# Kernel optimization log

Measured on AMD Instinct MI355X. Metric: run time of the kernel, lower is better.

The kernel has to match this reference:

```python
import jax, jax.numpy as jnp
import numpy as np

H = 128        # hidden_dim
R = 50         # num_rbf
L = 4          # num_layers
CUTOFF = 5.0
N = 10000      # atoms
M = 64         # molecules
BOX = 54.7     # box side -> ~32 neighbors within cutoff
EPS = 1e-5     # LayerNorm eps (torch default)


def setup_inputs() -> dict:
    rng = np.random.default_rng(0)
    positions = rng.uniform(0.0, BOX, size=(N, 3)).astype(np.float32)
    # static radius graph (the torch module filters a dense NxN pair list by cutoff;
    # we do that once here so runtime shapes are fixed / jit-friendly)
    sq = (positions ** 2).sum(-1)
    d2 = sq[:, None] + sq[None, :] - 2.0 * positions @ positions.T
    mask = (d2 < CUTOFF * CUTOFF) & ~np.eye(N, dtype=bool)
    row, col = np.nonzero(mask)
    edge_index = jnp.asarray(np.stack([row, col]).astype(np.int32))  # [2, E]

    key = jax.random.key(0)
    ks = jax.random.split(key, 6)
    s = 0.05
    return dict(
        atomic_numbers=jax.random.randint(ks[0], (N,), 0, 100),
        positions=jnp.asarray(positions),
        batch=jnp.asarray((np.arange(N) * M // N).astype(np.int32)),  # sorted, all M present
        edge_index=edge_index,
        embedding=jax.random.normal(ks[1], (100, H), jnp.float32) * s,
        W1=jax.random.normal(ks[2], (L, H + R, H), jnp.float32) * s,
        b1=jnp.zeros((L, H), jnp.float32),
        W2=jax.random.normal(ks[3], (L, H, H), jnp.float32) * s,
        b2=jnp.zeros((L, H), jnp.float32),
        W_ih=jax.random.normal(ks[4], (L, H, 3 * H), jnp.float32) * s,
        b_ih=jax.random.normal(ks[5], (L, 3 * H), jnp.float32) * s,
        b_hh=jnp.zeros((L, 3 * H), jnp.float32),
        ln_g=jnp.ones((H,), jnp.float32),
        ln_b=jnp.zeros((H,), jnp.float32),
    )


def reference(atomic_numbers, positions, batch, edge_index, embedding,
              W1, b1, W2, b2, W_ih, b_ih, b_hh, ln_g, ln_b):
    x = embedding[jnp.clip(atomic_numbers, 0, 99)]                  # [N, H]
    row, col = edge_index[0], edge_index[1]
    d = jnp.linalg.norm(positions[row] - positions[col], axis=-1)   # [E]
    centers = jnp.linspace(0.0, CUTOFF, R)
    width = CUTOFF / R
    rbf = jnp.exp(-((d[:, None] - centers) ** 2) / (2.0 * width * width))  # [E, R]
    n_atoms = x.shape[0]
    for l in range(L):
        x_j = x[row]                                                # gather [E, H]
        inp = jnp.concatenate([x_j, rbf], axis=-1)                  # [E, H+R]
        msg = jax.nn.silu(inp @ W1[l] + b1[l]) @ W2[l] + b2[l]      # [E, H]
        aggr = jax.ops.segment_sum(msg, col, num_segments=n_atoms)  # [N, H]
        # GRU step with h0 = 0: W_hh @ h vanishes, only b_hh survives
        gi = aggr @ W_ih[l] + b_ih[l]                               # [N, 3H]
        gi_r, gi_z, gi_n = jnp.split(gi, 3, axis=-1)
        bh_r, bh_z, bh_n = jnp.split(b_hh[l], 3)
        r = jax.nn.sigmoid(gi_r + bh_r)
        z = jax.nn.sigmoid(gi_z + bh_z)
        n = jnp.tanh(gi_n + r * bh_n)
        x = x + (1.0 - z) * n                                       # h' = (1-z)*n + z*0
    mu = x.mean(-1, keepdims=True)
    var = ((x - mu) ** 2).mean(-1, keepdims=True)
    x = (x - mu) / jnp.sqrt(var + EPS) * ln_g + ln_b
    sums = jax.ops.segment_sum(x, batch, num_segments=M)            # [M, H]
    counts = jax.ops.segment_sum(jnp.ones((x.shape[0],), jnp.float32), batch, num_segments=M)
    graph_rep = sums / jnp.clip(counts, 1.0)[:, None]
    return x, graph_rep
```

## Files before the change

kernel.cpp:

```cpp
#include <hip/hip_runtime.h>
#include <hip/hip_bf16.h>
#include <math.h>


#define HH 128
#define RR 50
#define LL 4
#define L2E 1.4426950408889634f

typedef __attribute__((ext_vector_type(8))) short short8;
typedef __attribute__((ext_vector_type(4))) float floatx4;

__device__ __forceinline__ unsigned short f2bf(float f) {
    unsigned u = __float_as_uint(f);
    unsigned r = (u + 0x7fffu + ((u >> 16) & 1u)) >> 16;
    return (unsigned short)r;
}
__device__ __forceinline__ unsigned pack_bf2(float lo, float hi) {
    unsigned u0 = __float_as_uint(lo) + 0x8000u;
    unsigned u1 = __float_as_uint(hi) + 0x8000u;
    return __builtin_amdgcn_perm(u1, u0, 0x07060302);
}
__device__ __forceinline__ float fast_sigmoid(float x) {
    return __builtin_amdgcn_rcpf(1.f + __builtin_amdgcn_exp2f(x * (-L2E)));
}
__device__ __forceinline__ float fast_tanh(float x) {
    x = fminf(fmaxf(x, -15.f), 15.f);
    float t = __builtin_amdgcn_exp2f(x * (2.f * L2E));
    return (t - 1.f) * __builtin_amdgcn_rcpf(t + 1.f);
}
__device__ __forceinline__ int imin(int a, int b) { return a < b ? a : b; }

__global__ __launch_bounds__(256) void prep_kernel(
    const int* __restrict__ an, const float* __restrict__ emb,
    float* __restrict__ X,
    const float* __restrict__ pos, const int* __restrict__ erow,
    const int* __restrict__ ecol, float* __restrict__ dist,
    int* __restrict__ rowptr, int* __restrict__ bptr,
    const int* __restrict__ batch,
    const float* __restrict__ W1, unsigned short* __restrict__ W1rT,
    unsigned short* __restrict__ W1xT,
    const float* __restrict__ W2, const float* __restrict__ Wih,
    unsigned short* __restrict__ WcT,
    const float* __restrict__ b2, float* __restrict__ P,
    const float* __restrict__ b1, unsigned short* __restrict__ embWbf,
    int* __restrict__ zc, float* __restrict__ outg,
    int N, int E, int M)
{
    int gidx = blockIdx.x * 256 + threadIdx.x;
    int c0 = N * HH;
    if (gidx < c0) {
        int i = gidx >> 7, n = gidx & 127;
        int z = an[i];
        z = z < 0 ? 0 : (z > 99 ? 99 : z);
        X[gidx] = emb[z * HH + n];
        return;
    }
    gidx -= c0;
    int PT = E > N ? E : N;
    if (gidx < PT) {
        int i = gidx;
        if (i < E) {
            int rc = erow[i];
            int rp = (i > 0) ? erow[i - 1] : -1;
            for (int r = rp + 1; r <= rc; ++r) rowptr[r] = i;
            if (i == E - 1)
                for (int r = rc + 1; r <= N; ++r) rowptr[r] = E;
        }
        if (i < N) {
            int bc = batch[i];
            int bp = (i > 0) ? batch[i - 1] : -1;
            for (int m = bp + 1; m <= bc; ++m) bptr[m] = i;
            if (i == N - 1)
                for (int m = bc + 1; m <= M; ++m) bptr[m] = N;
        }
        return;
    }
    gidx -= PT;
    if (gidx < E) {
        int e = gidx;
        int r = erow[e], c = ecol[e];
        float dx = pos[r * 3 + 0] - pos[c * 3 + 0];
        float dy = pos[r * 3 + 1] - pos[c * 3 + 1];
        float dz = pos[r * 3 + 2] - pos[c * 3 + 2];
        dist[e] = sqrtf(dx * dx + dy * dy + dz * dz);
        return;
    }
    gidx -= E;
    if (gidx < LL * HH * 64) {
        int l = gidx >> 13, rem = gidx & 8191;
        int f = rem >> 9, lane2 = (rem >> 3) & 63, j = rem & 7;
        int nt = f >> 1, h = f & 1;
        int n = nt * 16 + (lane2 & 15);
        int k = h * 32 + (lane2 >> 4) * 8 + j;
        float v = (k < RR) ? W1[((size_t)l * 178 + 128 + k) * HH + n] : 0.f;
        W1rT[gidx] = f2bf(v);
        return;
    }
    gidx -= LL * HH * 64;
    if (gidx < LL * HH * HH) {
        int l = gidx >> 14, rem = gidx & 16383, n = rem >> 7, k = rem & 127;
        W1xT[gidx] = f2bf(W1[((size_t)l * 178 + k) * HH + n]);
        return;
    }
    gidx -= LL * HH * HH;
    if (gidx < LL * HH * 384) {
        int l = gidx / (HH * 384), rem = gidx % (HH * 384);
        int i = rem / 384, j = rem % 384;
        const float* w2row = W2 + ((size_t)l * HH + i) * HH;
        const float* wih = Wih + (size_t)l * HH * 384;
        float acc = 0.f;
#pragma unroll 4
        for (int k = 0; k < HH; ++k)
            acc = fmaf(w2row[k], wih[(size_t)k * 384 + j], acc);
        WcT[((size_t)l * 384 + j) * HH + i] = f2bf(acc);
        return;
    }
    gidx -= LL * HH * 384;
    if (gidx < LL * 384) {
        int l = gidx / 384, j = gidx % 384;
        const float* b2l = b2 + (size_t)l * HH;
        const float* wih = Wih + (size_t)l * HH * 384;
        float acc = 0.f;
#pragma unroll 4
        for (int k = 0; k < HH; ++k)
            acc = fmaf(b2l[k], wih[(size_t)k * 384 + j], acc);
        P[gidx] = acc;
        return;
    }
    gidx -= LL * 384;
    if (gidx < N) {
        int z = an[gidx];
        zc[gidx] = z < 0 ? 0 : (z > 99 ? 99 : z);
        return;
    }
    gidx -= N;
    if (gidx < 100 * HH) {
        int z = gidx >> 7, n = gidx & 127;
        const float* er = emb + (size_t)z * HH;
        float acc = b1[n];
#pragma unroll 4
        for (int k = 0; k < HH; ++k)
            acc = fmaf(er[k], W1[(size_t)k * HH + n], acc);
        embWbf[gidx] = f2bf(acc);
        return;
    }
    gidx -= 100 * HH;
    if (gidx < M * HH) {
        outg[gidx] = 0.f;
    }
}

__global__ __launch_bounds__(256) void edge_mfma_kernel(
    const unsigned short* __restrict__ Xsrc, const unsigned short* __restrict__ W1rTf,
    const float* __restrict__ dist, const int* __restrict__ rowptr,
    const int* __restrict__ ecol, const int* __restrict__ zc, int use_z,
    unsigned short* __restrict__ Sbf, int N, int nwaves)
{
    __shared__ __align__(16) unsigned short W1s[8192];
    int tid = threadIdx.x;
    {
        const uint4* src = (const uint4*)W1rTf;
        uint4* dst = (uint4*)W1s;
#pragma unroll
        for (int i = 0; i < 4; ++i) dst[tid + i * 256] = src[tid + i * 256];
    }
    __syncthreads();

    int wid = (blockIdx.x << 2) + (tid >> 6);
    int lane = tid & 63;
    int c = lane & 15, q = lane >> 4;

    const float stepc = 5.0f / 49.0f;
    const float negc = -50.f * L2E;
    float kqs = (float)(q << 3) * stepc;

    int NW = 2 * N;
    for (int w = wid; w < NW; w += nwaves) {
        int a = w >> 1, h = w & 1;
        int es = rowptr[a], ee = rowptr[a + 1];
        float acc[4][4];
#pragma unroll
        for (int t = 0; t < 4; ++t)
#pragma unroll
            for (int r = 0; r < 4; ++r) acc[t][r] = 0.f;

        if (es < ee) {
            int last = ee - 1;
            int ce0 = imin(es + c, last);
            float dcur = dist[ce0];
            int c0raw = ecol[ce0];
            int rowcur = use_z ? zc[c0raw] : c0raw;
            int ce1 = imin(es + 16 + c, last);
            float dnxt = dist[ce1];
            int colnxt = ecol[ce1];

            for (int eb = es; eb < ee; eb += 16) {
                const unsigned short* xwrow = Xsrc + (size_t)rowcur * HH + h * 64;
                uint2 gx[4];
#pragma unroll
                for (int t = 0; t < 4; ++t)
                    gx[t] = *(const uint2*)&xwrow[t * 16 + (q << 2)];

                float d_t = dcur;
                dcur = dnxt;
                int rownxt = use_z ? zc[colnxt] : colnxt;
                int ce2 = imin(eb + 32 + c, last);
                dnxt = dist[ce2];
                colnxt = ecol[ce2];
                rowcur = rownxt;

                float dq0 = d_t - kqs;
                float dq1 = dq0 - 32.f * stepc;
                union { unsigned u[4]; short8 s; } ub0, ub1;
#pragma unroll
                for (int p = 0; p < 4; ++p) {
                    float t0 = dq0 - (float)(2 * p) * stepc;
                    float t1 = dq0 - (float)(2 * p + 1) * stepc;
                    float e0f = __builtin_amdgcn_exp2f(negc * t0 * t0);
                    float e1f = __builtin_amdgcn_exp2f(negc * t1 * t1);
                    ub0.u[p] = pack_bf2(e0f, e1f);
                    float t2 = dq1 - (float)(2 * p) * stepc;
                    float t3 = dq1 - (float)(2 * p + 1) * stepc;
                    float e2f = __builtin_amdgcn_exp2f(negc * t2 * t2);
                    float e3f = __builtin_amdgcn_exp2f(negc * t3 * t3);
                    ub1.u[p] = pack_bf2(e2f, e3f);
                }
                short8 B0 = ub0.s, B1 = ub1.s;
                float msk = ((eb + c) < ee) ? 1.f : 0.f;

                unsigned wbyte = (unsigned)(lane * 16);
                asm volatile("" : "+v"(wbyte));
                const char* Wlp = (const char*)W1s + wbyte;

#pragma unroll
                for (int t = 0; t < 4; ++t) {
                    int f0 = (h * 4 + t) * 2;
                    short8 A0 = *(const short8*)(Wlp + f0 * 1024);
                    short8 A1 = *(const short8*)(Wlp + (f0 + 1) * 1024);
                    floatx4 C;
                    C[0] = __uint_as_float(gx[t].x << 16);
                    C[1] = __uint_as_float(gx[t].x & 0xffff0000u);
                    C[2] = __uint_as_float(gx[t].y << 16);
                    C[3] = __uint_as_float(gx[t].y & 0xffff0000u);
                    C = __builtin_amdgcn_mfma_f32_16x16x32_bf16(A0, B0, C, 0, 0, 0);
                    C = __builtin_amdgcn_mfma_f32_16x16x32_bf16(A1, B1, C, 0, 0, 0);
#pragma unroll
                    for (int r = 0; r < 4; ++r) {
                        float hh = C[r];
                        float v = hh * fast_sigmoid(hh);
                        acc[t][r] = fmaf(v, msk, acc[t][r]);
                    }
                }
            }
        }

        int b0 = c & 1, b1 = (c >> 1) & 1, b2 = (c >> 2) & 1, b3 = (c >> 3) & 1;
        float s1[4][2];
#pragma unroll
        for (int t = 0; t < 4; ++t)
#pragma unroll
            for (int p = 0; p < 2; ++p) {
                float keep = b0 ? acc[t][2 * p + 1] : acc[t][2 * p];
                float send = b0 ? acc[t][2 * p] : acc[t][2 * p + 1];
                s1[t][p] = keep + __shfl_xor(send, 1, 64);
            }
        float s2[4];
#pragma unroll
        for (int t = 0; t < 4; ++t) {
            float keep = b1 ? s1[t][1] : s1[t][0];
            float send = b1 ? s1[t][0] : s1[t][1];
            s2[t] = keep + __shfl_xor(send, 2, 64);
        }
        float s3[2];
#pragma unroll
        for (int u = 0; u < 2; ++u) {
            float keep = b2 ? s2[2 * u + 1] : s2[2 * u];
            float send = b2 ? s2[2 * u] : s2[2 * u + 1];
            s3[u] = keep + __shfl_xor(send, 4, 64);
        }
        float keep = b3 ? s3[1] : s3[0];
        float send = b3 ? s3[0] : s3[1];
        float fin = keep + __shfl_xor(send, 8, 64);

        int t_fin = 2 * b3 + b2;
        int r_fin = 2 * b1 + b0;
        int n = t_fin * 16 + (q << 2) + r_fin;
        Sbf[(size_t)a * HH + h * 64 + n] = f2bf(fin);
    }
}

#define GA 32
__global__ __launch_bounds__(256) void grux_mfma_kernel(
    const unsigned short* __restrict__ Sbf, const unsigned short* __restrict__ WcT,
    const float* __restrict__ P, const float* __restrict__ bih,
    const float* __restrict__ bhh, const int* __restrict__ rowptr,
    float* __restrict__ X, int N,
    const unsigned short* __restrict__ W1xT, const float* __restrict__ b1next,
    unsigned short* __restrict__ XWb, int do_xw,
    int do_ln, const float* __restrict__ lng, const float* __restrict__ lnb,
    const int* __restrict__ batch, const int* __restrict__ bptr,
    float* __restrict__ outx, float* __restrict__ outg)
{
    __shared__ __align__(16) union ShMem {
        struct { unsigned short Sb[GA][136]; unsigned short Xb[GA][136]; } s;
        struct { float Xf[GA][132]; float pool[2][HH]; } f;
    } u;
    unsigned short (&Sb)[GA][136] = u.s.Sb;
    unsigned short (&Xb)[GA][136] = u.s.Xb;
    float (&Xf)[GA][132] = u.f.Xf;
    float (&pool)[2][HH] = u.f.pool;

    int tid = threadIdx.x;
    int abase = blockIdx.x * GA;
    int w = tid >> 6, lane = tid & 63, c = lane & 15, q = lane >> 4;

    float pn[2][3], bi[2][3], bh[2][3], deg[2][4];
#pragma unroll
    for (int t = 0; t < 2; ++t) {
        int n = w * 32 + t * 16 + c;
#pragma unroll
        for (int g = 0; g < 3; ++g) {
            pn[t][g] = P[g * 128 + n];
            bi[t][g] = bih[g * 128 + n];
            bh[t][g] = bhh[g * 128 + n];
        }
    }
#pragma unroll
    for (int sub = 0; sub < 2; ++sub)
#pragma unroll
        for (int r = 0; r < 4; ++r) {
            int a = abase + sub * 16 + q * 4 + r;
            deg[sub][r] = (a < N) ? (float)(rowptr[a + 1] - rowptr[a]) : 0.f;
        }

    {
        int a = tid >> 3, ch = tid & 7;
        int aa = abase + a; if (aa >= N) aa = N - 1;
        const uint4* src = (const uint4*)(Sbf + (size_t)aa * HH + ch * 16);
        uint4 v0 = src[0];
        uint4 v1 = src[1];
        uint4* dst = (uint4*)&Sb[a][ch * 16];
        dst[0] = v0;
        dst[1] = v1;
    }
    __syncthreads();

    floatx4 Cg[3][2][2];
#pragma unroll
    for (int g = 0; g < 3; ++g)
#pragma unroll
        for (int t = 0; t < 2; ++t)
#pragma unroll
            for (int sub = 0; sub < 2; ++sub)
                Cg[g][t][sub] = floatx4{0.f, 0.f, 0.f, 0.f};

#pragma unroll
    for (int kt = 0; kt < 4; ++kt) {
        short8 A0 = *(const short8*)&Sb[c][kt * 32 + q * 8];
        short8 A1 = *(const short8*)&Sb[16 + c][kt * 32 + q * 8];
#pragma unroll
        for (int g = 0; g < 3; ++g)
#pragma unroll
            for (int t = 0; t < 2; ++t) {
                int nrow = g * 128 + w * 32 + t * 16 + c;
                short8 B = *(const short8*)&WcT[(size_t)nrow * HH + kt * 32 + q * 8];
                Cg[g][t][0] = __builtin_amdgcn_mfma_f32_16x16x32_bf16(A0, B, Cg[g][t][0], 0, 0, 0);
                Cg[g][t][1] = __builtin_amdgcn_mfma_f32_16x16x32_bf16(A1, B, Cg[g][t][1], 0, 0, 0);
            }
    }

    if (do_ln) __syncthreads();

#pragma unroll
    for (int sub = 0; sub < 2; ++sub)
#pragma unroll
        for (int r = 0; r < 4; ++r) {
            int am = sub * 16 + q * 4 + r;
            int a = abase + am;
            bool ok = a < N;
#pragma unroll
            for (int t = 0; t < 2; ++t) {
                int n = w * 32 + t * 16 + c;
                float g0 = Cg[0][t][sub][r] + deg[sub][r] * pn[t][0] + bi[t][0];
                float g1 = Cg[1][t][sub][r] + deg[sub][r] * pn[t][1] + bi[t][1];
                float g2 = Cg[2][t][sub][r] + deg[sub][r] * pn[t][2] + bi[t][2];
                float rr = fast_sigmoid(g0 + bh[t][0]);
                float zz = fast_sigmoid(g1 + bh[t][1]);
                float nn = fast_tanh(g2 + rr * bh[t][2]);
                float xv = 0.f;
                if (ok) {
                    xv = X[(size_t)a * HH + n] + (1.f - zz) * nn;
                    if (!do_ln) X[(size_t)a * HH + n] = xv;
                }
                if (do_ln) Xf[am][n] = xv;
                else       Xb[am][n] = f2bf(xv);
            }
        }

    if (do_ln) {
        (&pool[0][0])[tid] = 0.f;
        __syncthreads();

        int row = tid >> 3, j = tid & 7;
        int a2 = abase + row;
        float4 x0 = *(const float4*)&Xf[row][j * 16];
        float4 x1 = *(const float4*)&Xf[row][j * 16 + 4];
        float4 x2 = *(const float4*)&Xf[row][j * 16 + 8];
        float4 x3 = *(const float4*)&Xf[row][j * 16 + 12];
        float s = x0.x + x0.y + x0.z + x0.w + x1.x + x1.y + x1.z + x1.w
                + x2.x + x2.y + x2.z + x2.w + x3.x + x3.y + x3.z + x3.w;
        s += __shfl_xor(s, 1, 64);
        s += __shfl_xor(s, 2, 64);
        s += __shfl_xor(s, 4, 64);
        float mu = s * (1.f / 128.f);
        float qv = 0.f;
#define QACC(v) { float dx=(v).x-mu, dy=(v).y-mu, dz=(v).z-mu, dw=(v).w-mu; \
                  qv += dx*dx + dy*dy + dz*dz + dw*dw; }
        QACC(x0) QACC(x1) QACC(x2) QACC(x3)
#undef QACC
        qv += __shfl_xor(qv, 1, 64);
        qv += __shfl_xor(qv, 2, 64);
        qv += __shfl_xor(qv, 4, 64);
        float inv = rsqrtf(qv * (1.f / 128.f) + 1e-5f);

        int m0 = batch[abase];
        if (a2 < N) {
            int midx = batch[a2] - m0;
            const float4* gg = (const float4*)&lng[j * 16];
            const float4* bb = (const float4*)&lnb[j * 16];
            float* outrow = outx + (size_t)a2 * HH + j * 16;
            float* pl = &pool[midx][j * 16];
            float4 xs[4] = {x0, x1, x2, x3};
#pragma unroll
            for (int i = 0; i < 4; ++i) {
                float4 gv = gg[i], bv = bb[i], xv4 = xs[i];
                float4 y;
                y.x = (xv4.x - mu) * inv * gv.x + bv.x;
                y.y = (xv4.y - mu) * inv * gv.y + bv.y;
                y.z = (xv4.z - mu) * inv * gv.z + bv.z;
                y.w = (xv4.w - mu) * inv * gv.w + bv.w;
                *(float4*)(outrow + i * 4) = y;
                atomicAdd(pl + i * 4 + 0, y.x);
                atomicAdd(pl + i * 4 + 1, y.y);
                atomicAdd(pl + i * 4 + 2, y.z);
                atomicAdd(pl + i * 4 + 3, y.w);
            }
        }
        __syncthreads();

        int a_last = abase + GA - 1; if (a_last >= N) a_last = N - 1;
        int mlast = batch[a_last];
        int mi = tid >> 7, col = tid & 127;
        int m = m0 + mi;
        if (m <= mlast) {
            float cnt = (float)(bptr[m + 1] - bptr[m]);
            float invc = 1.f / fmaxf(cnt, 1.f);
            atomicAdd(&outg[(size_t)m * HH + col], pool[mi][col] * invc);
        }
        return;
    }

    if (!do_xw) return;
    __syncthreads();

    floatx4 Cx[2][2];
#pragma unroll
    for (int t = 0; t < 2; ++t)
#pragma unroll
        for (int sub = 0; sub < 2; ++sub)
            Cx[t][sub] = floatx4{0.f, 0.f, 0.f, 0.f};
#pragma unroll
    for (int kt = 0; kt < 4; ++kt) {
        short8 A0 = *(const short8*)&Xb[c][kt * 32 + q * 8];
        short8 A1 = *(const short8*)&Xb[16 + c][kt * 32 + q * 8];
#pragma unroll
        for (int t = 0; t < 2; ++t) {
            int nrow = w * 32 + t * 16 + c;
            short8 B = *(const short8*)&W1xT[(size_t)nrow * HH + kt * 32 + q * 8];
            Cx[t][0] = __builtin_amdgcn_mfma_f32_16x16x32_bf16(A0, B, Cx[t][0], 0, 0, 0);
            Cx[t][1] = __builtin_amdgcn_mfma_f32_16x16x32_bf16(A1, B, Cx[t][1], 0, 0, 0);
        }
    }
#pragma unroll
    for (int sub = 0; sub < 2; ++sub)
#pragma unroll
        for (int r = 0; r < 4; ++r) {
            int a = abase + sub * 16 + q * 4 + r;
            if (a >= N) continue;
#pragma unroll
            for (int t = 0; t < 2; ++t) {
                int n = w * 32 + t * 16 + c;
                XWb[(size_t)a * HH + n] = f2bf(Cx[t][sub][r] + b1next[n]);
            }
        }
}

extern "C" void kernel_launch(void* const* d_in, const int* in_sizes, int n_in,
                              void* d_out, int out_size, void* d_ws, size_t ws_size,
                              hipStream_t stream)
{
    const int*   an   = (const int*)d_in[0];
    const float* pos  = (const float*)d_in[1];
    const int*   bat  = (const int*)d_in[2];
    const int*   eidx = (const int*)d_in[3];
    const float* emb  = (const float*)d_in[4];
    const float* W1   = (const float*)d_in[5];
    const float* b1   = (const float*)d_in[6];
    const float* W2   = (const float*)d_in[7];
    const float* b2   = (const float*)d_in[8];
    const float* Wih  = (const float*)d_in[9];
    const float* bih  = (const float*)d_in[10];
    const float* bhh  = (const float*)d_in[11];
    const float* lng  = (const float*)d_in[12];
    const float* lnb  = (const float*)d_in[13];

    int N = in_sizes[0];
    int E = in_sizes[3] / 2;
    int M = out_size / HH - N;
    const int* erow = eidx;
    const int* ecol = eidx + E;

    float* ws   = (float*)d_ws;
    size_t off = 0;
    float* X    = ws + off; off += (size_t)N * HH;
    unsigned short* Sbf = (unsigned short*)(ws + off); off += (size_t)N * HH / 2;
    unsigned short* XWb = (unsigned short*)(ws + off); off += (size_t)N * HH / 2;
    float* P    = ws + off; off += LL * 384;
    float* dist = ws + off; off += E;
    int* rowptr = (int*)(ws + off); off += N + 1;
    int* bptr   = (int*)(ws + off); off += M + 1;
    off = (off + 3) & ~(size_t)3;
    unsigned short* W1rT = (unsigned short*)(ws + off); off += (size_t)LL * HH * 32;
    unsigned short* W1xT = (unsigned short*)(ws + off); off += (size_t)LL * HH * 64;
    unsigned short* WcT  = (unsigned short*)(ws + off); off += (size_t)LL * 384 * 64;
    unsigned short* embWbf = (unsigned short*)(ws + off); off += (size_t)100 * HH / 2;
    int* zc     = (int*)(ws + off); off += N;

    float* outx = (float*)d_out;
    float* outg = outx + (size_t)N * HH;

    int PT = (E > N ? E : N);
    long total = (long)N * HH + PT + E + LL * HH * 64 + LL * HH * HH
               + LL * HH * 384 + LL * 384 + N + 100 * HH + (long)M * HH;
    int prep_blocks = (int)((total + 255) / 256);

    prep_kernel<<<prep_blocks, 256, 0, stream>>>(
        an, emb, X, pos, erow, ecol, dist, rowptr, bptr, bat,
        W1, W1rT, W1xT, W2, Wih, WcT, b2, P,
        b1, embWbf, zc, outg, N, E, M);

    int eblocks = (2 * N + 3) / 4;
    int nwaves = eblocks * 4;
    int grux_blocks = (N + GA - 1) / GA;
    for (int l = 0; l < LL; ++l) {
        edge_mfma_kernel<<<eblocks, 256, 0, stream>>>(
            (l == 0) ? embWbf : XWb, W1rT + (size_t)l * HH * 64,
            dist, rowptr, ecol, zc, (l == 0) ? 1 : 0, Sbf, N, nwaves);
        int do_xw = (l < LL - 1) ? 1 : 0;
        int do_ln = (l == LL - 1) ? 1 : 0;
        int ln = (l + 1 < LL) ? l + 1 : l;
        grux_mfma_kernel<<<grux_blocks, 256, 0, stream>>>(
            Sbf, WcT + (size_t)l * 384 * HH, P + l * 384,
            bih + l * 384, bhh + l * 384, rowptr, X, N,
            W1xT + (size_t)ln * HH * HH, b1 + (size_t)ln * HH, XWb, do_xw,
            do_ln, lng, lnb, bat, bptr, outx, outg);
    }
}
```

Measured before the change: 305.5 us.

## Fuse edge message kernel and GRU update into one per-layer kernel

Merges the per-atom edge aggregation kernel and the GRU/next-layer projection kernel into a single layer kernel that processes 16 atoms per block. Aggregated messages now stay in shared memory instead of round-tripping through a global bf16 buffer. XW output is double-buffered across layers so a layer can read the previous projection while writing the next. The cost is smaller GRU MFMA tiles (16 atoms instead of 32), which halves reuse of the WcT/W1xT loads from global memory. Every block also reloads the W1 slice into shared memory, and there are 8 wave-tasks per block over 4 waves, which can cause load imbalance.

```diff
diff --git a/kernel.cpp b/kernel.cpp
--- a/kernel.cpp
+++ b/kernel.cpp
@@ -6,6 +6,7 @@
 #define HH 128
 #define RR 50
 #define LL 4
+#define GA 16
 #define L2E 1.4426950408889634f
 
 typedef __attribute__((ext_vector_type(8))) short short8;
@@ -151,13 +152,29 @@
     }
 }
 
-__global__ __launch_bounds__(256) void edge_mfma_kernel(
+__global__ __launch_bounds__(256) void layer_kernel(
     const unsigned short* __restrict__ Xsrc, const unsigned short* __restrict__ W1rTf,
     const float* __restrict__ dist, const int* __restrict__ rowptr,
     const int* __restrict__ ecol, const int* __restrict__ zc, int use_z,
-    unsigned short* __restrict__ Sbf, int N, int nwaves)
+    const unsigned short* __restrict__ WcT, const float* __restrict__ P,
+    const float* __restrict__ bih, const float* __restrict__ bhh,
+    float* __restrict__ X, int N,
+    const unsigned short* __restrict__ W1xT, const float* __restrict__ b1next,
+    unsigned short* __restrict__ XWout, int do_xw,
+    int do_ln, const float* __restrict__ lng, const float* __restrict__ lnb,
+    const int* __restrict__ batch, const int* __restrict__ bptr,
+    float* __restrict__ outx, float* __restrict__ outg)
 {
     __shared__ __align__(16) unsigned short W1s[8192];
+    __shared__ __align__(16) union ShMem {
+        struct { unsigned short Sb[GA][136]; unsigned short Xb[GA][136]; } s;
+        struct { float Xf[GA][132]; float pool[2][HH]; } f;
+    } sh;
+    unsigned short (&Sb)[GA][136] = sh.s.Sb;
+    unsigned short (&Xb)[GA][136] = sh.s.Xb;
+    float (&Xf)[GA][132] = sh.f.Xf;
+    float (&pool)[2][HH] = sh.f.pool;
+
     int tid = threadIdx.x;
     {
         const uint4* src = (const uint4*)W1rTf;
@@ -167,18 +184,20 @@
     }
     __syncthreads();
 
-    int wid = (blockIdx.x << 2) + (tid >> 6);
-    int lane = tid & 63;
+    int abase = blockIdx.x * GA;
+    int wavei = tid >> 6, lane = tid & 63;
     int c = lane & 15, q = lane >> 4;
 
     const float stepc = 5.0f / 49.0f;
     const float negc = -50.f * L2E;
     float kqs = (float)(q << 3) * stepc;
 
-    int NW = 2 * N;
-    for (int w = wid; w < NW; w += nwaves) {
-        int a = w >> 1, h = w & 1;
-        int es = rowptr[a], ee = rowptr[a + 1];
+#pragma unroll 1
+    for (int uu = wavei; uu < 2 * GA; uu += 4) {
+        int a_loc = uu >> 1, h = uu & 1;
+        int a = abase + a_loc;
+        int es = 0, ee = 0;
+        if (a < N) { es = rowptr[a]; ee = rowptr[a + 1]; }
         float acc[4][4];
 #pragma unroll
         for (int t = 0; t < 4; ++t)
@@ -247,8 +266,8 @@
                     C = __builtin_amdgcn_mfma_f32_16x16x32_bf16(A1, B1, C, 0, 0, 0);
 #pragma unroll
                     for (int r = 0; r < 4; ++r) {
-                        float hh = C[r];
-                        float v = hh * fast_sigmoid(hh);
+                        float hh2 = C[r];
+                        float v = hh2 * fast_sigmoid(hh2);
                         acc[t][r] = fmaf(v, msk, acc[t][r]);
                     }
                 }
@@ -274,10 +293,10 @@
         }
         float s3[2];
 #pragma unroll
-        for (int u = 0; u < 2; ++u) {
-            float keep = b2 ? s2[2 * u + 1] : s2[2 * u];
-            float send = b2 ? s2[2 * u] : s2[2 * u + 1];
-            s3[u] = keep + __shfl_xor(send, 4, 64);
+        for (int u2 = 0; u2 < 2; ++u2) {
+            float keep = b2 ? s2[2 * u2 + 1] : s2[2 * u2];
+            float send = b2 ? s2[2 * u2] : s2[2 * u2 + 1];
+            s3[u2] = keep + __shfl_xor(send, 4, 64);
         }
         float keep = b3 ? s3[1] : s3[0];
         float send = b3 ? s3[0] : s3[1];
@@ -286,39 +305,15 @@
         int t_fin = 2 * b3 + b2;
         int r_fin = 2 * b1 + b0;
         int n = t_fin * 16 + (q << 2) + r_fin;
-        Sbf[(size_t)a * HH + h * 64 + n] = f2bf(fin);
-    }
-}
-
-#define GA 32
-__global__ __launch_bounds__(256) void grux_mfma_kernel(
-    const unsigned short* __restrict__ Sbf, const unsigned short* __restrict__ WcT,
-    const float* __restrict__ P, const float* __restrict__ bih,
-    const float* __restrict__ bhh, const int* __restrict__ rowptr,
-    float* __restrict__ X, int N,
-    const unsigned short* __restrict__ W1xT, const float* __restrict__ b1next,
-    unsigned short* __restrict__ XWb, int do_xw,
-    int do_ln, const float* __restrict__ lng, const float* __restrict__ lnb,
-    const int* __restrict__ batch, const int* __restrict__ bptr,
-    float* __restrict__ outx, float* __restrict__ outg)
-{
-    __shared__ __align__(16) union ShMem {
-        struct { unsigned short Sb[GA][136]; unsigned short Xb[GA][136]; } s;
-        struct { float Xf[GA][132]; float pool[2][HH]; } f;
-    } u;
-    unsigned short (&Sb)[GA][136] = u.s.Sb;
-    unsigned short (&Xb)[GA][136] = u.s.Xb;
-    float (&Xf)[GA][132] = u.f.Xf;
-    float (&pool)[2][HH] = u.f.pool;
-
-    int tid = threadIdx.x;
-    int abase = blockIdx.x * GA;
-    int w = tid >> 6, lane = tid & 63, c = lane & 15, q = lane >> 4;
-
-    float pn[2][3], bi[2][3], bh[2][3], deg[2][4];
+        Sb[a_loc][h * 64 + n] = f2bf(fin);
+    }
+    __syncthreads();
+
+    int wq = wavei;
+    float pn[2][3], bi[2][3], bh[2][3], deg[4];
 #pragma unroll
     for (int t = 0; t < 2; ++t) {
-        int n = w * 32 + t * 16 + c;
+        int n = wq * 32 + t * 16 + c;
 #pragma unroll
         for (int g = 0; g < 3; ++g) {
             pn[t][g] = P[g * 128 + n];
@@ -327,113 +322,92 @@
         }
     }
 #pragma unroll
-    for (int sub = 0; sub < 2; ++sub)
-#pragma unroll
-        for (int r = 0; r < 4; ++r) {
-            int a = abase + sub * 16 + q * 4 + r;
-            deg[sub][r] = (a < N) ? (float)(rowptr[a + 1] - rowptr[a]) : 0.f;
-        }
-
-    {
-        int a = tid >> 3, ch = tid & 7;
-        int aa = abase + a; if (aa >= N) aa = N - 1;
-        const uint4* src = (const uint4*)(Sbf + (size_t)aa * HH + ch * 16);
-        uint4 v0 = src[0];
-        uint4 v1 = src[1];
-        uint4* dst = (uint4*)&Sb[a][ch * 16];
-        dst[0] = v0;
-        dst[1] = v1;
-    }
-    __syncthreads();
-
-    floatx4 Cg[3][2][2];
+    for (int r = 0; r < 4; ++r) {
+        int a = abase + q * 4 + r;
+        deg[r] = (a < N) ? (float)(rowptr[a + 1] - rowptr[a]) : 0.f;
+    }
+
+    floatx4 Cg[3][2];
 #pragma unroll
     for (int g = 0; g < 3; ++g)
 #pragma unroll
         for (int t = 0; t < 2; ++t)
-#pragma unroll
-            for (int sub = 0; sub < 2; ++sub)
-                Cg[g][t][sub] = floatx4{0.f, 0.f, 0.f, 0.f};
+            Cg[g][t] = floatx4{0.f, 0.f, 0.f, 0.f};
 
 #pragma unroll
     for (int kt = 0; kt < 4; ++kt) {
         short8 A0 = *(const short8*)&Sb[c][kt * 32 + q * 8];
-        short8 A1 = *(const short8*)&Sb[16 + c][kt * 32 + q * 8];
 #pragma unroll
         for (int g = 0; g < 3; ++g)
 #pragma unroll
             for (int t = 0; t < 2; ++t) {
-                int nrow = g * 128 + w * 32 + t * 16 + c;
+                int nrow = g * 128 + wq * 32 + t * 16 + c;
                 short8 B = *(const short8*)&WcT[(size_t)nrow * HH + kt * 32 + q * 8];
-                Cg[g][t][0] = __builtin_amdgcn_mfma_f32_16x16x32_bf16(A0, B, Cg[g][t][0], 0, 0, 0);
-                Cg[g][t][1] = __builtin_amdgcn_mfma_f32_16x16x32_bf16(A1, B, Cg[g][t][1], 0, 0, 0);
+                Cg[g][t] = __builtin_amdgcn_mfma_f32_16x16x32_bf16(A0, B, Cg[g][t], 0, 0, 0);
             }
     }
 
     if (do_ln) __syncthreads();
 
 #pragma unroll
-    for (int sub = 0; sub < 2; ++sub)
-#pragma unroll
-        for (int r = 0; r < 4; ++r) {
-            int am = sub * 16 + q * 4 + r;
-            int a = abase + am;
-            bool ok = a < N;
-#pragma unroll
-            for (int t = 0; t < 2; ++t) {
-                int n = w * 32 + t * 16 + c;
-                float g0 = Cg[0][t][sub][r] + deg[sub][r] * pn[t][0] + bi[t][0];
-                float g1 = Cg[1][t][sub][r] + deg[sub][r] * pn[t][1] + bi[t][1];
-                float g2 = Cg[2][t][sub][r] + deg[sub][r] * pn[t][2] + bi[t][2];
-                float rr = fast_sigmoid(g0 + bh[t][0]);
-                float zz = fast_sigmoid(g1 + bh[t][1]);
-                float nn = fast_tanh(g2 + rr * bh[t][2]);
-                float xv = 0.f;
-                if (ok) {
-                    xv = X[(size_t)a * HH + n] + (1.f - zz) * nn;
-                    if (!do_ln) X[(size_t)a * HH + n] = xv;
-                }
-                if (do_ln) Xf[am][n] = xv;
-                else       Xb[am][n] = f2bf(xv);
+    for (int r = 0; r < 4; ++r) {
+        int am = q * 4 + r;
+        int a = abase + am;
+        bool ok = a < N;
+#pragma unroll
+        for (int t = 0; t < 2; ++t) {
+            int n = wq * 32 + t * 16 + c;
+            float g0 = Cg[0][t][r] + deg[r] * pn[t][0] + bi[t][0];
+            float g1 = Cg[1][t][r] + deg[r] * pn[t][1] + bi[t][1];
+            float g2 = Cg[2][t][r] + deg[r] * pn[t][2] + bi[t][2];
+            float rr = fast_sigmoid(g0 + bh[t][0]);
+            float zz = fast_sigmoid(g1 + bh[t][1]);
+            float nn = fast_tanh(g2 + rr * bh[t][2]);
+            float xv = 0.f;
+            if (ok) {
+                xv = X[(size_t)a * HH + n] + (1.f - zz) * nn;
+                if (!do_ln) X[(size_t)a * HH + n] = xv;
             }
-        }
+            if (do_ln) Xf[am][n] = xv;
+            else       Xb[am][n] = f2bf(xv);
+        }
+    }
 
     if (do_ln) {
         (&pool[0][0])[tid] = 0.f;
         __syncthreads();
 
-        int row = tid >> 3, j = tid & 7;
+        int row = tid >> 4, j = tid & 15;
         int a2 = abase + row;
-        float4 x0 = *(const float4*)&Xf[row][j * 16];
-        float4 x1 = *(const float4*)&Xf[row][j * 16 + 4];
-        float4 x2 = *(const float4*)&Xf[row][j * 16 + 8];
-        float4 x3 = *(const float4*)&Xf[row][j * 16 + 12];
-        float s = x0.x + x0.y + x0.z + x0.w + x1.x + x1.y + x1.z + x1.w
-                + x2.x + x2.y + x2.z + x2.w + x3.x + x3.y + x3.z + x3.w;
+        float4 x0 = *(const float4*)&Xf[row][j * 8];
+        float4 x1 = *(const float4*)&Xf[row][j * 8 + 4];
+        float s = x0.x + x0.y + x0.z + x0.w + x1.x + x1.y + x1.z + x1.w;
         s += __shfl_xor(s, 1, 64);
         s += __shfl_xor(s, 2, 64);
         s += __shfl_xor(s, 4, 64);
+        s += __shfl_xor(s, 8, 64);
         float mu = s * (1.f / 128.f);
         float qv = 0.f;
 #define QACC(v) { float dx=(v).x-mu, dy=(v).y-mu, dz=(v).z-mu, dw=(v).w-mu; \
                   qv += dx*dx + dy*dy + dz*dz + dw*dw; }
-        QACC(x0) QACC(x1) QACC(x2) QACC(x3)
+        QACC(x0) QACC(x1)
 #undef QACC
         qv += __shfl_xor(qv, 1, 64);
         qv += __shfl_xor(qv, 2, 64);
         qv += __shfl_xor(qv, 4, 64);
+        qv += __shfl_xor(qv, 8, 64);
         float inv = rsqrtf(qv * (1.f / 128.f) + 1e-5f);
 
         int m0 = batch[abase];
         if (a2 < N) {
             int midx = batch[a2] - m0;
-            const float4* gg = (const float4*)&lng[j * 16];
-            const float4* bb = (const float4*)&lnb[j * 16];
-            float* outrow = outx + (size_t)a2 * HH + j * 16;
-            float* pl = &pool[midx][j * 16];
-            float4 xs[4] = {x0, x1, x2, x3};
-#pragma unroll
-            for (int i = 0; i < 4; ++i) {
+            const float4* gg = (const float4*)&lng[j * 8];
+            const float4* bb = (const float4*)&lnb[j * 8];
+            float* outrow = outx + (size_t)a2 * HH + j * 8;
+            float* pl = &pool[midx][j * 8];
+            float4 xs[2] = {x0, x1};
+#pragma unroll
+            for (int i = 0; i < 2; ++i) {
                 float4 gv = gg[i], bv = bb[i], xv4 = xs[i];
                 float4 y;
                 y.x = (xv4.x - mu) * inv * gv.x + bv.x;
@@ -464,36 +438,30 @@
     if (!do_xw) return;
     __syncthreads();
 
-    floatx4 Cx[2][2];
+    floatx4 Cx[2];
 #pragma unroll
     for (int t = 0; t < 2; ++t)
-#pragma unroll
-        for (int sub = 0; sub < 2; ++sub)
-            Cx[t][sub] = floatx4{0.f, 0.f, 0.f, 0.f};
+        Cx[t] = floatx4{0.f, 0.f, 0.f, 0.f};
 #pragma unroll
     for (int kt = 0; kt < 4; ++kt) {
         short8 A0 = *(const short8*)&Xb[c][kt * 32 + q * 8];
-        short8 A1 = *(const short8*)&Xb[16 + c][kt * 32 + q * 8];
 #pragma unroll
         for (int t = 0; t < 2; ++t) {
-            int nrow = w * 32 + t * 16 + c;
+            int nrow = wq * 32 + t * 16 + c;
             short8 B = *(const short8*)&W1xT[(size_t)nrow * HH + kt * 32 + q * 8];
-            Cx[t][0] = __builtin_amdgcn_mfma_f32_16x16x32_bf16(A0, B, Cx[t][0], 0, 0, 0);
-            Cx[t][1] = __builtin_amdgcn_mfma_f32_16x16x32_bf16(A1, B, Cx[t][1], 0, 0, 0);
-        }
-    }
-#pragma unroll
-    for (int sub = 0; sub < 2; ++sub)
-#pragma unroll
-        for (int r = 0; r < 4; ++r) {
-            int a = abase + sub * 16 + q * 4 + r;
-            if (a >= N) continue;
-#pragma unroll
-            for (int t = 0; t < 2; ++t) {
-                int n = w * 32 + t * 16 + c;
-                XWb[(size_t)a * HH + n] = f2bf(Cx[t][sub][r] + b1next[n]);
-            }
-        }
+            Cx[t] = __builtin_amdgcn_mfma_f32_16x16x32_bf16(A0, B, Cx[t], 0, 0, 0);
+        }
+    }
+#pragma unroll
+    for (int r = 0; r < 4; ++r) {
+        int a = abase + q * 4 + r;
+        if (a >= N) continue;
+#pragma unroll
+        for (int t = 0; t < 2; ++t) {
+            int n = wq * 32 + t * 16 + c;
+            XWout[(size_t)a * HH + n] = f2bf(Cx[t][r] + b1next[n]);
+        }
+    }
 }
 
 extern "C" void kernel_launch(void* const* d_in, const int* in_sizes, int n_in,
@@ -524,8 +492,8 @@
     float* ws   = (float*)d_ws;
     size_t off = 0;
     float* X    = ws + off; off += (size_t)N * HH;
-    unsigned short* Sbf = (unsigned short*)(ws + off); off += (size_t)N * HH / 2;
-    unsigned short* XWb = (unsigned short*)(ws + off); off += (size_t)N * HH / 2;
+    unsigned short* XWb0 = (unsigned short*)(ws + off); off += (size_t)N * HH / 2;
+    unsigned short* XWb1 = (unsigned short*)(ws + off); off += (size_t)N * HH / 2;
     float* P    = ws + off; off += LL * 384;
     float* dist = ws + off; off += E;
     int* rowptr = (int*)(ws + off); off += N + 1;
@@ -550,20 +518,20 @@
         W1, W1rT, W1xT, W2, Wih, WcT, b2, P,
         b1, embWbf, zc, outg, N, E, M);
 
-    int eblocks = (2 * N + 3) / 4;
-    int nwaves = eblocks * 4;
-    int grux_blocks = (N + GA - 1) / GA;
+    int nb = (N + GA - 1) / GA;
+    unsigned short* xwbuf[2] = {XWb0, XWb1};
     for (int l = 0; l < LL; ++l) {
-        edge_mfma_kernel<<<eblocks, 256, 0, stream>>>(
-            (l == 0) ? embWbf : XWb, W1rT + (size_t)l * HH * 64,
-            dist, rowptr, ecol, zc, (l == 0) ? 1 : 0, Sbf, N, nwaves);
+        const unsigned short* src = (l == 0) ? embWbf : xwbuf[(l + 1) & 1];
+        unsigned short* dst = xwbuf[l & 1];
         int do_xw = (l < LL - 1) ? 1 : 0;
         int do_ln = (l == LL - 1) ? 1 : 0;
         int ln = (l + 1 < LL) ? l + 1 : l;
-        grux_mfma_kernel<<<grux_blocks, 256, 0, stream>>>(
-            Sbf, WcT + (size_t)l * 384 * HH, P + l * 384,
-            bih + l * 384, bhh + l * 384, rowptr, X, N,
-            W1xT + (size_t)ln * HH * HH, b1 + (size_t)ln * HH, XWb, do_xw,
+        layer_kernel<<<nb, 256, 0, stream>>>(
+            src, W1rT + (size_t)l * HH * 64, dist, rowptr, ecol, zc,
+            (l == 0) ? 1 : 0,
+            WcT + (size_t)l * 384 * HH, P + l * 384,
+            bih + l * 384, bhh + l * 384, X, N,
+            W1xT + (size_t)ln * HH * HH, b1 + (size_t)ln * HH, dst, do_xw,
             do_ln, lng, lnb, bat, bptr, outx, outg);
     }
 }
```

Result: slower. 327.7 us (+7.3%).
